# Performance work log

Measured on AMD Instinct MI355X. Metric: run time of the kernel, lower is better.

Reference implementation:

```python
import jax, jax.numpy as jnp
import numpy as np

B, S, D, H = 2, 2048, 1024, 16
DK = D // H


def setup_inputs() -> dict:
    key = jax.random.key(0)
    ks = jax.random.split(key, 11)
    scale = 1.0 / np.sqrt(D)
    inp = {
        "k": jax.random.normal(ks[0], (B, S, D), jnp.float32),
        "q": jax.random.normal(ks[1], (B, S, D), jnp.float32),
        "v": jax.random.normal(ks[2], (B, S, D), jnp.float32),
        "w_q": jax.random.normal(ks[3], (D, D), jnp.float32) * scale,
        "b_q": jax.random.normal(ks[4], (D,), jnp.float32) * 0.01,
        "w_k": jax.random.normal(ks[5], (D, D), jnp.float32) * scale,
        "b_k": jax.random.normal(ks[6], (D,), jnp.float32) * 0.01,
        "w_v": jax.random.normal(ks[7], (D, D), jnp.float32) * scale,
        "b_v": jax.random.normal(ks[8], (D,), jnp.float32) * 0.01,
        "w_o": jax.random.normal(ks[9], (D, D), jnp.float32) * scale,
        "b_o": jax.random.normal(ks[10], (D,), jnp.float32) * 0.01,
        # causal mask; positions with mask==0 get -1e9 (masked_fill semantics)
        "mask": jnp.tril(jnp.ones((1, 1, S, S), jnp.int32)),
    }
    return inp


def reference(k, q, v, w_q, b_q, w_k, b_k, w_v, b_v, w_o, b_o, mask):
    MINUS_INF = -1000000000.0

    def proj(x, w, b):
        # nn.Linear: x @ w.T + b, then split heads -> [B, H, S, DK]
        y = x @ w.T + b
        return y.reshape(B, S, H, DK).transpose(0, 2, 1, 3)

    Q = proj(q, w_q, b_q)
    K = proj(k, w_k, b_k)
    V = proj(v, w_v, b_v)

    # [B, H, Sq, Sk] scores
    scores = jnp.einsum("bhqd,bhkd->bhqk", Q, K) / jnp.sqrt(jnp.float32(DK))
    scores = jnp.where(mask == 0, MINUS_INF, scores)
    attn = jax.nn.softmax(scores, axis=-1)

    out = jnp.einsum("bhqk,bhkd->bhqd", attn, V)  # [B, H, S, DK]
    out = out.transpose(0, 2, 1, 3).reshape(B, S, D)  # concat heads
    return out @ w_o.T + b_o
```

## Files before the change

### kernel.cpp

```cpp
#include <hip/hip_runtime.h>

typedef __bf16 bf16;
typedef __bf16 v8bf __attribute__((ext_vector_type(8)));
typedef __bf16 v4bf __attribute__((ext_vector_type(4)));
typedef float  v4f  __attribute__((ext_vector_type(4)));

#define MFMA16(a,b,c) __builtin_amdgcn_mfma_f32_16x16x32_bf16((a),(b),(c),0,0,0)

static constexpr int Sq = 2048;
static constexpr size_t NI = 4194304;
static constexpr size_t NW = 1048576;

__device__ __forceinline__ void gld_lds16(const void* g, void* l) {
  __builtin_amdgcn_global_load_lds(
      (__attribute__((address_space(1))) unsigned int*)g,
      (__attribute__((address_space(3))) unsigned int*)l,
      16, 0, 0);
}

__device__ __forceinline__ float exp2_raw(float x) {
  return __builtin_amdgcn_exp2f(x);
}

__global__ __launch_bounds__(256) void convert_kernel(
    const float* __restrict__ q, const float* __restrict__ k, const float* __restrict__ v,
    const float* __restrict__ wq, const float* __restrict__ wk,
    const float* __restrict__ wv, const float* __restrict__ wo,
    bf16* __restrict__ dst)
{
  const int NI4 = 1048576;
  const int NW4 = 262144;
  int idx = blockIdx.x * 256 + threadIdx.x;
  const float* src; size_t dstoff; int local;
  if (idx < 3 * NI4) {
    int a = idx >> 20; local = idx & (NI4 - 1);
    src = (a == 0) ? q : ((a == 1) ? k : v);
    dstoff = (size_t)a * NI;
  } else {
    int t = idx - 3 * NI4;
    int a = t >> 18; local = t & (NW4 - 1);
    src = (a == 0) ? wq : ((a == 1) ? wk : ((a == 2) ? wv : wo));
    dstoff = 3 * NI + (size_t)a * NW;
  }
  float4 f = ((const float4*)src)[local];
  v4bf hv = { (bf16)f.x, (bf16)f.y, (bf16)f.z, (bf16)f.w };
  *(v4bf*)(dst + dstoff + (size_t)local * 4) = hv;
}

__device__ __forceinline__ void gemm_bt_body(
    const bf16* __restrict__ A, const bf16* __restrict__ Bw,
    const float* __restrict__ bias, bf16* __restrict__ outh,
    int bm, int bn, int mode)
{
  __shared__ alignas(16) bf16 As[128 * 32];
  __shared__ alignas(16) bf16 Bs[128 * 32];
  const int tid = threadIdx.x;
  const int wave = tid >> 6, lane = tid & 63;
  const int quad = lane >> 4, l15 = lane & 15;
  const int wm = (wave >> 1) * 64, wn = (wave & 1) * 64;
  const int lrow = lane >> 2, lcol = (lane & 3) * 8;

  v4f acc[4][4];
#pragma unroll
  for (int i = 0; i < 4; i++)
#pragma unroll
    for (int j = 0; j < 4; j++) { v4f z = {0.f, 0.f, 0.f, 0.f}; acc[i][j] = z; }

  const bf16* gA = A  + (size_t)(bm + wave * 32 + lrow) * 1024 + lcol;
  const bf16* gB = Bw + (size_t)(bn + wave * 32 + lrow) * 1024 + lcol;
  bf16* lA0 = &As[(wave * 32) * 32];
  bf16* lA1 = &As[(wave * 32 + 16) * 32];
  bf16* lB0 = &Bs[(wave * 32) * 32];
  bf16* lB1 = &Bs[(wave * 32 + 16) * 32];

  for (int k0 = 0; k0 < 1024; k0 += 32) {
    gld_lds16(gA + k0, lA0);
    gld_lds16(gA + 16 * 1024 + k0, lA1);
    gld_lds16(gB + k0, lB0);
    gld_lds16(gB + 16 * 1024 + k0, lB1);
    __syncthreads();
    v8bf af[4], bfr[4];
#pragma unroll
    for (int i = 0; i < 4; i++)
      af[i] = *(const v8bf*)&As[(wm + i * 16 + l15) * 32 + quad * 8];
#pragma unroll
    for (int j = 0; j < 4; j++)
      bfr[j] = *(const v8bf*)&Bs[(wn + j * 16 + l15) * 32 + quad * 8];
#pragma unroll
    for (int i = 0; i < 4; i++)
#pragma unroll
      for (int j = 0; j < 4; j++)
        acc[i][j] = MFMA16(af[i], bfr[j], acc[i][j]);
    __syncthreads();
  }

#pragma unroll
  for (int i = 0; i < 4; i++) {
    const int m0 = bm + wm + i * 16 + quad * 4;
#pragma unroll
    for (int j = 0; j < 4; j++) {
      const int n = bn + wn + j * 16 + l15;
      const float bv = bias[n];
      if (mode == 2) {
        int b_ = m0 >> 11, s_ = m0 & 2047;
        int h_ = n >> 6,  dk = n & 63;
        v4bf pk;
#pragma unroll
        for (int r = 0; r < 4; r++) pk[r] = (bf16)(acc[i][j][r] + bv);
        *(v4bf*)&outh[((size_t)((b_ * 16 + h_) * 64 + dk)) * 2048 + s_] = pk;
      } else {
        const float sc = (mode == 3) ? 0.18033688011112042f : 1.0f;
        int h_ = n >> 6,  dk = n & 63;
#pragma unroll
        for (int r = 0; r < 4; r++) {
          int m = m0 + r;
          int b_ = m >> 11, s_ = m & 2047;
          outh[(((size_t)(b_ * 16 + h_) * 2048 + s_) << 6) + dk] =
              (bf16)((acc[i][j][r] + bv) * sc);
        }
      }
    }
  }
}

__global__ __launch_bounds__(256, 2) void gemm_proj_kernel(
    const bf16* qb, const bf16* kb, const bf16* vb,
    const bf16* wqb, const bf16* wkb, const bf16* wvb,
    const float* bq, const float* bk, const float* bv,
    bf16* Qh, bf16* Kh, bf16* VhT)
{
  const bf16* A; const bf16* W; const float* bias; bf16* out; int mode;
  if (blockIdx.z == 0)      { A = qb; W = wqb; bias = bq; out = Qh;  mode = 3; }
  else if (blockIdx.z == 1) { A = kb; W = wkb; bias = bk; out = Kh;  mode = 0; }
  else                      { A = vb; W = wvb; bias = bv; out = VhT; mode = 2; }
  gemm_bt_body(A, W, bias, out, blockIdx.y * 128, blockIdx.x * 128, mode);
}

__global__ __launch_bounds__(256, 4) void gemm_final_kernel(
    const bf16* __restrict__ Ob, const bf16* __restrict__ wob,
    const float* __restrict__ bo, float* __restrict__ out)
{
  __shared__ alignas(16) bf16 As[64 * 32];
  __shared__ alignas(16) bf16 Bs[128 * 32];
  const int bm = blockIdx.y * 64, bn = blockIdx.x * 128;
  const int tid = threadIdx.x;
  const int wave = tid >> 6, lane = tid & 63;
  const int quad = lane >> 4, l15 = lane & 15;
  const int wm = (wave >> 1) * 32, wn = (wave & 1) * 64;
  const int lrow = lane >> 2, lcol = (lane & 3) * 8;

  v4f acc[2][4];
#pragma unroll
  for (int i = 0; i < 2; i++)
#pragma unroll
    for (int j = 0; j < 4; j++) { v4f z = {0.f, 0.f, 0.f, 0.f}; acc[i][j] = z; }

  const bf16* gA = Ob  + (size_t)(bm + wave * 16 + lrow) * 1024 + lcol;
  const bf16* gB = wob + (size_t)(bn + wave * 32 + lrow) * 1024 + lcol;
  bf16* lA  = &As[(wave * 16) * 32];
  bf16* lB0 = &Bs[(wave * 32) * 32];
  bf16* lB1 = &Bs[(wave * 32 + 16) * 32];

  for (int k0 = 0; k0 < 1024; k0 += 32) {
    gld_lds16(gA + k0, lA);
    gld_lds16(gB + k0, lB0);
    gld_lds16(gB + 16 * 1024 + k0, lB1);
    __syncthreads();
    v8bf af[2], bfr[4];
#pragma unroll
    for (int i = 0; i < 2; i++)
      af[i] = *(const v8bf*)&As[(wm + i * 16 + l15) * 32 + quad * 8];
#pragma unroll
    for (int j = 0; j < 4; j++)
      bfr[j] = *(const v8bf*)&Bs[(wn + j * 16 + l15) * 32 + quad * 8];
#pragma unroll
    for (int i = 0; i < 2; i++)
#pragma unroll
      for (int j = 0; j < 4; j++)
        acc[i][j] = MFMA16(af[i], bfr[j], acc[i][j]);
    __syncthreads();
  }

#pragma unroll
  for (int i = 0; i < 2; i++) {
    const int m0 = bm + wm + i * 16 + quad * 4;
#pragma unroll
    for (int j = 0; j < 4; j++) {
      const int n = bn + wn + j * 16 + l15;
      const float bv = bo[n];
#pragma unroll
      for (int r = 0; r < 4; r++)
        out[(size_t)(m0 + r) * 1024 + n] = acc[i][j][r] + bv;
    }
  }
}

__global__ __launch_bounds__(128, 2) void attn_kernel(
    const bf16* __restrict__ Qh, const bf16* __restrict__ Kh,
    const bf16* __restrict__ VhT, bf16* __restrict__ Ob)
{
  __shared__ alignas(16) bf16 Ps[2][32 * 72];
  const int tid = threadIdx.x;
  const int wave = tid >> 6, lane = tid & 63;
  const int quad = lane >> 4, l15 = lane & 15;
  const int bh = blockIdx.x, gy = blockIdx.y;
  const int b = bh >> 4, h = bh & 15;
  const int r8 = gy & 7, q8 = gy >> 3;
  const int u = 8 * q8 + ((q8 & 1) ? (7 - r8) : r8);
  const int qt = 2 * u + wave;
  const int L = u;
  const bf16* Qb = Qh + (size_t)bh * Sq * 64;
  const bf16* Kb = Kh + (size_t)bh * Sq * 64;
  const bf16* Vb = VhT + (size_t)bh * 64 * Sq;
  bf16* Pw = &Ps[wave][0];
  const int r0 = qt * 32;

  v8bf aq[2][2];
#pragma unroll
  for (int s = 0; s < 2; s++)
#pragma unroll
    for (int ks = 0; ks < 2; ks++)
      aq[s][ks] = *(const v8bf*)&Qb[(size_t)(r0 + s * 16 + l15) * 64 + ks * 32 + quad * 8];

  float lsumT[2];
  v4f o[2][4];
  lsumT[0] = 0.f; lsumT[1] = 0.f;
#pragma unroll
  for (int s = 0; s < 2; s++)
#pragma unroll
    for (int j = 0; j < 4; j++) { v4f z = {0.f, 0.f, 0.f, 0.f}; o[s][j] = z; }

  auto loadK = [&](int kb, v8bf (&BK)[4][2]) {
#pragma unroll
    for (int n = 0; n < 4; n++) {
      BK[n][0] = *(const v8bf*)&Kb[(size_t)(kb + n * 16 + l15) * 64 + quad * 8];
      BK[n][1] = *(const v8bf*)&Kb[(size_t)(kb + n * 16 + l15) * 64 + 32 + quad * 8];
    }
  };
  auto loadV = [&](int kb, v8bf (&BV)[4][2]) {
#pragma unroll
    for (int n = 0; n < 4; n++) {
      BV[n][0] = *(const v8bf*)&Vb[(size_t)(n * 16 + l15) * 2048 + kb + quad * 8];
      BV[n][1] = *(const v8bf*)&Vb[(size_t)(n * 16 + l15) * 2048 + kb + 32 + quad * 8];
    }
  };
  auto compute = [&](const v8bf (&BK)[4][2], const v8bf (&BV)[4][2], int kc, bool diag) {
    const int kbase = kc * 64;
#pragma unroll
    for (int s = 0; s < 2; s++) {
      v4f cnT[4];
#pragma unroll
      for (int n = 0; n < 4; n++) {
        v4f z = {0.f, 0.f, 0.f, 0.f};
        cnT[n] = MFMA16(BK[n][0], aq[s][0], z);
        cnT[n] = MFMA16(BK[n][1], aq[s][1], cnT[n]);
      }
      const int qglob = r0 + s * 16 + l15;
#pragma unroll
      for (int n = 0; n < 4; n++) {
        const int kb_n = kbase + n * 16 + quad * 4;
        v4bf pk;
#pragma unroll
        for (int r = 0; r < 4; r++) {
          float e = exp2_raw(cnT[n][r]);
          if (diag && (kb_n + r) > qglob) e = 0.f;
          lsumT[s] += e;
          pk[r] = (bf16)e;
        }
        *(v4bf*)&Pw[(s * 16 + l15) * 72 + n * 16 + quad * 4] = pk;
      }
    }
#pragma unroll
    for (int s = 0; s < 2; s++) {
      v8bf ap0 = *(const v8bf*)&Pw[(s * 16 + l15) * 72 + quad * 8];
      v8bf ap1 = *(const v8bf*)&Pw[(s * 16 + l15) * 72 + 32 + quad * 8];
#pragma unroll
      for (int j = 0; j < 4; j++) {
        o[s][j] = MFMA16(ap0, BV[j][0], o[s][j]);
        o[s][j] = MFMA16(ap1, BV[j][1], o[s][j]);
      }
    }
  };

  v8bf bk0[4][2], bk1[4][2], bvv[4][2];
  loadK(0, bk0);
  int kc = 0;
  while (kc < L) {
    loadV(kc * 64, bvv);
    loadK((kc + 1) * 64, bk1);
    compute(bk0, bvv, kc, false);
    ++kc;
    if (kc >= L) {
      loadV(kc * 64, bvv);
      compute(bk1, bvv, kc, true);
      kc = -1;
      break;
    }
    loadV(kc * 64, bvv);
    loadK((kc + 1) * 64, bk0);
    compute(bk1, bvv, kc, false);
    ++kc;
  }
  if (kc >= 0) {
    loadV(kc * 64, bvv);
    compute(bk0, bvv, kc, true);
  }

#pragma unroll
  for (int s = 0; s < 2; s++) {
    lsumT[s] += __shfl_xor(lsumT[s], 16, 64);
    lsumT[s] += __shfl_xor(lsumT[s], 32, 64);
  }
#pragma unroll
  for (int s = 0; s < 2; s++) {
    float inv[4];
#pragma unroll
    for (int r = 0; r < 4; r++)
      inv[r] = 1.0f / __shfl(lsumT[s], quad * 4 + r, 64);
#pragma unroll
    for (int r = 0; r < 4; r++) {
      const int sg = r0 + s * 16 + quad * 4 + r;
#pragma unroll
      for (int j = 0; j < 4; j++)
        Ob[((size_t)(b * Sq + sg)) * 1024 + h * 64 + j * 16 + l15] =
            (bf16)(o[s][j][r] * inv[r]);
    }
  }
}

extern "C" void kernel_launch(void* const* d_in, const int* in_sizes, int n_in,
                              void* d_out, int out_size, void* d_ws, size_t ws_size,
                              hipStream_t stream) {
  (void)in_sizes; (void)n_in; (void)out_size; (void)ws_size;
  const float* kin = (const float*)d_in[0];
  const float* qin = (const float*)d_in[1];
  const float* vin = (const float*)d_in[2];
  const float* wq  = (const float*)d_in[3];
  const float* bq  = (const float*)d_in[4];
  const float* wk  = (const float*)d_in[5];
  const float* bk  = (const float*)d_in[6];
  const float* wv  = (const float*)d_in[7];
  const float* bv  = (const float*)d_in[8];
  const float* wo  = (const float*)d_in[9];
  const float* bo  = (const float*)d_in[10];

  bf16* ws = (bf16*)d_ws;
  bf16* qb  = ws;
  bf16* kb  = ws + NI;
  bf16* vb  = ws + 2 * NI;
  bf16* wqb = ws + 3 * NI;
  bf16* wkb = wqb + NW;
  bf16* wvb = wqb + 2 * NW;
  bf16* wob = wqb + 3 * NW;
  bf16* Qh  = ws + 3 * NI + 4 * NW;
  bf16* Kh  = Qh + NI;
  bf16* VhT = Qh + 2 * NI;
  bf16* Ob  = Qh + 3 * NI;

  convert_kernel<<<16384, 256, 0, stream>>>(qin, kin, vin, wq, wk, wv, wo, ws);
  gemm_proj_kernel<<<dim3(8, 32, 3), 256, 0, stream>>>(
      qb, kb, vb, wqb, wkb, wvb, bq, bk, bv, Qh, Kh, VhT);
  attn_kernel<<<dim3(32, 32), 128, 0, stream>>>(Qh, Kh, VhT, Ob);
  gemm_final_kernel<<<dim3(8, 64), 256, 0, stream>>>(Ob, wob, bo, (float*)d_out);
}
```

Before: 251.8 us.

## Split long causal attention rows across two blocks and combine partials

The attention grid grows from 32 to 48 slots per head. Query tiles in the upper half, which have the longest causal key ranges, are split into two key-range halves. Each half writes unnormalized bf16 partial outputs and row sums to workspace, and a new combine kernel adds them and normalizes. The occupancy hint also rises from 2 to 3 blocks per SIMD. This is meant to balance the triangular workload and raise parallelism, at the cost of an extra launch, extra global traffic, and bf16 rounding of the partials.

Result: slower. 305.7 us (+21.4%).

```diff
diff --git a/kernel.cpp b/kernel.cpp
--- a/kernel.cpp
+++ b/kernel.cpp
@@ -195,20 +195,35 @@
   }
 }
 
-__global__ __launch_bounds__(128, 2) void attn_kernel(
+__global__ __launch_bounds__(128, 3) void attn_kernel(
     const bf16* __restrict__ Qh, const bf16* __restrict__ Kh,
-    const bf16* __restrict__ VhT, bf16* __restrict__ Ob)
+    const bf16* __restrict__ VhT, bf16* __restrict__ Ob,
+    bf16* __restrict__ po, float* __restrict__ plsum)
 {
   __shared__ alignas(16) bf16 Ps[2][32 * 72];
   const int tid = threadIdx.x;
   const int wave = tid >> 6, lane = tid & 63;
   const int quad = lane >> 4, l15 = lane & 15;
-  const int bh = blockIdx.x, gy = blockIdx.y;
+  const int bh = blockIdx.x, slot = blockIdx.y;
   const int b = bh >> 4, h = bh & 15;
-  const int r8 = gy & 7, q8 = gy >> 3;
-  const int u = 8 * q8 + ((q8 & 1) ? (7 - r8) : r8);
-  const int qt = 2 * u + wave;
-  const int L = u;
+
+  int t, lo, part;
+  if (slot < 16) {
+    t = (slot < 8) ? slot : 23 - slot;
+    lo = 0; part = -1;
+  } else if (slot < 32) {
+    int c = slot - 16;
+    t = 16 + ((c < 8) ? c : 23 - c);
+    lo = 0; part = 0;
+  } else {
+    int c = slot - 32;
+    t = 16 + ((c < 8) ? c : 23 - c);
+    lo = 16; part = 1;
+  }
+  const int qt = 2 * t + wave;
+  const int L = t;
+  const int hi = (part == 0) ? 15 : t;
+
   const bf16* Qb = Qh + (size_t)bh * Sq * 64;
   const bf16* Kb = Kh + (size_t)bh * Sq * 64;
   const bf16* Vb = VhT + (size_t)bh * 64 * Sq;
@@ -282,28 +297,30 @@
     }
   };
 
-  v8bf bk0[4][2], bk1[4][2], bvv[4][2];
-  loadK(0, bk0);
-  int kc = 0;
-  while (kc < L) {
-    loadV(kc * 64, bvv);
-    loadK((kc + 1) * 64, bk1);
-    compute(bk0, bvv, kc, false);
-    ++kc;
-    if (kc >= L) {
+  {
+    v8bf bk0[4][2], bk1[4][2], bvv[4][2];
+    loadK(lo * 64, bk0);
+    int kc = lo;
+    while (kc < hi) {
       loadV(kc * 64, bvv);
-      compute(bk1, bvv, kc, true);
-      kc = -1;
-      break;
-    }
-    loadV(kc * 64, bvv);
-    loadK((kc + 1) * 64, bk0);
-    compute(bk1, bvv, kc, false);
-    ++kc;
-  }
-  if (kc >= 0) {
-    loadV(kc * 64, bvv);
-    compute(bk0, bvv, kc, true);
+      loadK((kc + 1) * 64, bk1);
+      compute(bk0, bvv, kc, false);
+      ++kc;
+      if (kc >= hi) {
+        loadV(kc * 64, bvv);
+        compute(bk1, bvv, kc, kc == L);
+        kc = -1;
+        break;
+      }
+      loadV(kc * 64, bvv);
+      loadK((kc + 1) * 64, bk0);
+      compute(bk1, bvv, kc, false);
+      ++kc;
+    }
+    if (kc >= 0) {
+      loadV(kc * 64, bvv);
+      compute(bk0, bvv, kc, kc == L);
+    }
   }
 
 #pragma unroll
@@ -311,20 +328,60 @@
     lsumT[s] += __shfl_xor(lsumT[s], 16, 64);
     lsumT[s] += __shfl_xor(lsumT[s], 32, 64);
   }
-#pragma unroll
-  for (int s = 0; s < 2; s++) {
-    float inv[4];
-#pragma unroll
-    for (int r = 0; r < 4; r++)
-      inv[r] = 1.0f / __shfl(lsumT[s], quad * 4 + r, 64);
-#pragma unroll
-    for (int r = 0; r < 4; r++) {
-      const int sg = r0 + s * 16 + quad * 4 + r;
+
+  if (part < 0) {
+#pragma unroll
+    for (int s = 0; s < 2; s++) {
+      float inv[4];
+#pragma unroll
+      for (int r = 0; r < 4; r++)
+        inv[r] = 1.0f / __shfl(lsumT[s], quad * 4 + r, 64);
+#pragma unroll
+      for (int r = 0; r < 4; r++) {
+        const int sg = r0 + s * 16 + quad * 4 + r;
+#pragma unroll
+        for (int j = 0; j < 4; j++)
+          Ob[((size_t)(b * Sq + sg)) * 1024 + h * 64 + j * 16 + l15] =
+              (bf16)(o[s][j][r] * inv[r]);
+      }
+    }
+  } else {
+    const size_t pidx = ((size_t)(bh * 32 + (qt - 32)) * 2 + part);
+    bf16* pob = po + pidx * 2048;
+#pragma unroll
+    for (int s = 0; s < 2; s++)
 #pragma unroll
       for (int j = 0; j < 4; j++)
-        Ob[((size_t)(b * Sq + sg)) * 1024 + h * 64 + j * 16 + l15] =
-            (bf16)(o[s][j][r] * inv[r]);
-    }
+#pragma unroll
+        for (int r = 0; r < 4; r++)
+          pob[(s * 16 + quad * 4 + r) * 64 + j * 16 + l15] = (bf16)o[s][j][r];
+    if (quad == 0) {
+#pragma unroll
+      for (int s = 0; s < 2; s++)
+        plsum[pidx * 32 + s * 16 + l15] = lsumT[s];
+    }
+  }
+}
+
+__global__ __launch_bounds__(256) void attn_combine_kernel(
+    const bf16* __restrict__ po, const float* __restrict__ plsum,
+    bf16* __restrict__ Ob)
+{
+  const int bh = blockIdx.x, ti = blockIdx.y;
+  const int b = bh >> 4, h = bh & 15;
+  const int tid = threadIdx.x;
+  const int col = tid & 63, rg = tid >> 6;
+  const size_t pidx = (size_t)(bh * 32 + ti) * 2;
+  const bf16* p0 = po + pidx * 2048;
+  const bf16* p1 = p0 + 2048;
+  const float* l0 = plsum + pidx * 32;
+#pragma unroll
+  for (int rr = 0; rr < 8; rr++) {
+    const int row = rg * 8 + rr;
+    const float inv = 1.0f / (l0[row] + l0[32 + row]);
+    const float v = (float)p0[row * 64 + col] + (float)p1[row * 64 + col];
+    const int sg = (32 + ti) * 32 + row;
+    Ob[((size_t)(b * 2048 + sg)) * 1024 + h * 64 + col] = (bf16)(v * inv);
   }
 }
 
@@ -356,10 +413,13 @@
   bf16* Kh  = Qh + NI;
   bf16* VhT = Qh + 2 * NI;
   bf16* Ob  = Qh + 3 * NI;
+  bf16*  po    = Ob + NI;
+  float* plsum = (float*)(po + (size_t)32 * 32 * 2 * 2048);
 
   convert_kernel<<<16384, 256, 0, stream>>>(qin, kin, vin, wq, wk, wv, wo, ws);
   gemm_proj_kernel<<<dim3(8, 32, 3), 256, 0, stream>>>(
       qb, kb, vb, wqb, wkb, wvb, bq, bk, bv, Qh, Kh, VhT);
-  attn_kernel<<<dim3(32, 32), 128, 0, stream>>>(Qh, Kh, VhT, Ob);
+  attn_kernel<<<dim3(32, 48), 128, 0, stream>>>(Qh, Kh, VhT, Ob, po, plsum);
+  attn_combine_kernel<<<dim3(32, 32), 256, 0, stream>>>(po, plsum, Ob);
   gemm_final_kernel<<<dim3(8, 64), 256, 0, stream>>>(Ob, wob, bo, (float*)d_out);
 }
```
